# Kernel tuning notes

Measured on AMD Instinct MI355X. Metric: run time of the kernel, lower is better.

The kernel has to match this reference:

```python
import jax, jax.numpy as jnp
from jax import lax
import numpy as np

H = 161  # input_size == hidden_size per the torch module


def _lstm(x, w_ih, w_hh, b_ih, b_hh, reverse):
    """Single-direction LSTM matching torch.nn.LSTM gate order (i, f, g, o).
    x: [B, T, I] -> returns hidden states [B, T, H]."""
    # Precompute the input contribution for all timesteps in one GEMM.
    pre = jnp.einsum('bti,gi->btg', x, w_ih) + b_ih + b_hh  # [B, T, 4H]
    B = x.shape[0]

    def step(carry, p):
        h, c = carry
        gates = p + h @ w_hh.T  # [B, 4H]
        i, f, g, o = jnp.split(gates, 4, axis=-1)
        c = jax.nn.sigmoid(f) * c + jax.nn.sigmoid(i) * jnp.tanh(g)
        h = jax.nn.sigmoid(o) * jnp.tanh(c)
        return (h, c), h

    init = (jnp.zeros((B, H), x.dtype), jnp.zeros((B, H), x.dtype))
    _, hs = lax.scan(step, init, jnp.swapaxes(pre, 0, 1), reverse=reverse)
    return jnp.swapaxes(hs, 0, 1)  # [B, T, H]


def _block(h, p, relu):
    # p = (wih_f, whh_f, bih_f, bhh_f, wih_b, whh_b, bih_b, bhh_b, W, b)
    f = _lstm(h, p[0], p[1], p[2], p[3], reverse=False)
    b = _lstm(h, p[4], p[5], p[6], p[7], reverse=True)
    out = jnp.concatenate([f, b], axis=-1) @ p[8].T + p[9]  # Linear(2H -> H)
    if relu:
        out = jax.nn.relu(out)
    return out + h  # residual


def _forward(x, p1, p2, p3):
    h = _block(x, p1, relu=True)
    h = _block(h, p2, relu=True)
    h = _block(h, p3, relu=False)  # block 3: no ReLU before residual in the torch code
    return h


def setup_inputs() -> dict:
    key = jax.random.key(0)
    ks = iter(jax.random.split(key, 64))
    s = 1.0 / np.sqrt(H)  # torch LSTM/Linear default uniform init scale

    def u(shape):
        return jax.random.uniform(next(ks), shape, jnp.float32, -s, s)

    inp = {"x": jax.random.normal(next(ks), (32, 1000, H), jnp.float32)}
    shapes = [("wih_f", (4 * H, H)), ("whh_f", (4 * H, H)), ("bih_f", (4 * H,)), ("bhh_f", (4 * H,)),
              ("wih_b", (4 * H, H)), ("whh_b", (4 * H, H)), ("bih_b", (4 * H,)), ("bhh_b", (4 * H,)),
              ("W", (H, 2 * H)), ("bl", (H,))]
    for i in (1, 2, 3):
        for nm, sh in shapes:
            inp[f"l{i}_{nm}"] = u(sh)
    return inp


def reference(x,
              l1_wih_f, l1_whh_f, l1_bih_f, l1_bhh_f, l1_wih_b, l1_whh_b, l1_bih_b, l1_bhh_b, l1_W, l1_bl,
              l2_wih_f, l2_whh_f, l2_bih_f, l2_bhh_f, l2_wih_b, l2_whh_b, l2_bih_b, l2_bhh_b, l2_W, l2_bl,
              l3_wih_f, l3_whh_f, l3_bih_f, l3_bhh_f, l3_wih_b, l3_whh_b, l3_bih_b, l3_bhh_b, l3_W, l3_bl):
    p1 = (l1_wih_f, l1_whh_f, l1_bih_f, l1_bhh_f, l1_wih_b, l1_whh_b, l1_bih_b, l1_bhh_b, l1_W, l1_bl)
    p2 = (l2_wih_f, l2_whh_f, l2_bih_f, l2_bhh_f, l2_wih_b, l2_whh_b, l2_bih_b, l2_bhh_b, l2_W, l2_bl)
    p3 = (l3_wih_f, l3_whh_f, l3_bih_f, l3_bhh_f, l3_wih_b, l3_whh_b, l3_bih_b, l3_bhh_b, l3_W, l3_bl)
    return _forward(x, p1, p2, p3)
```

## Files before the change

kernel.cpp:

```cpp
#include <hip/hip_runtime.h>
#include <hip/hip_fp16.h>

#define H 161
#define G4 644
#define BB 32
#define TT 1000
#define M_TOT (BB*TT)
#define KXP 192
#define KLP 352
#define NWIH 1344
#define NPAIR 84
#define NVEC (NPAIR/4)

typedef _Float16 h2_t  __attribute__((ext_vector_type(2)));
typedef _Float16 f16x8 __attribute__((ext_vector_type(8)));
typedef float    f32x4 __attribute__((ext_vector_type(4)));

__device__ __forceinline__ h2_t bc_h2(unsigned int u) {
    return __builtin_bit_cast(h2_t, u);
}

__device__ __forceinline__ float dot2f(h2_t a, h2_t b, float c) {
#if __has_builtin(__builtin_amdgcn_fdot2)
    return __builtin_amdgcn_fdot2(a, b, c, false);
#else
    return c + (float)a[0] * (float)b[0] + (float)a[1] * (float)b[1];
#endif
}

__device__ __forceinline__ float tanh_f(float x) {
    return 1.0f - 2.0f / (__expf(2.0f * x) + 1.0f);
}

__device__ __forceinline__ void bar_lds() {
    __builtin_amdgcn_sched_barrier(0);
    asm volatile("s_waitcnt lgkmcnt(0)" ::: "memory");
    __builtin_amdgcn_s_barrier();
    __builtin_amdgcn_sched_barrier(0);
}

__global__ __launch_bounds__(256) void cvt_x(
    const float* __restrict__ in,
    __half* __restrict__ out)
{
    const int total = M_TOT * KXP;
    for (int idx = blockIdx.x * 256 + threadIdx.x; idx < total;
         idx += gridDim.x * 256) {
        int m = idx / KXP, k = idx - m * KXP;
        float v = (k < H) ? in[(size_t)m * H + k] : (k == H ? 1.f : 0.f);
        out[idx] = __float2half(v);
    }
}

__global__ __launch_bounds__(256) void cvt_wih3(
    const float* __restrict__ wf0, const float* __restrict__ wb0,
    const float* __restrict__ bif0, const float* __restrict__ bhf0,
    const float* __restrict__ bib0, const float* __restrict__ bhb0,
    const float* __restrict__ wf1, const float* __restrict__ wb1,
    const float* __restrict__ bif1, const float* __restrict__ bhf1,
    const float* __restrict__ bib1, const float* __restrict__ bhb1,
    const float* __restrict__ wf2, const float* __restrict__ wb2,
    const float* __restrict__ bif2, const float* __restrict__ bhf2,
    const float* __restrict__ bib2, const float* __restrict__ bhb2,
    __half* __restrict__ out)
{
    const int l = blockIdx.y;
    const float* wf  = (l == 0) ? wf0  : (l == 1) ? wf1  : wf2;
    const float* wb  = (l == 0) ? wb0  : (l == 1) ? wb1  : wb2;
    const float* bif = (l == 0) ? bif0 : (l == 1) ? bif1 : bif2;
    const float* bhf = (l == 0) ? bhf0 : (l == 1) ? bhf1 : bhf2;
    const float* bib = (l == 0) ? bib0 : (l == 1) ? bib1 : bib2;
    const float* bhb = (l == 0) ? bhb0 : (l == 1) ? bhb1 : bhb2;
    __half* o = out + (size_t)l * NWIH * KXP;

    const int total = NWIH * KXP;
    for (int idx = blockIdx.x * 256 + threadIdx.x; idx < total;
         idx += gridDim.x * 256) {
        int n = idx / KXP, k = idx - n * KXP;
        float v = 0.f;
        if (n < G4) {
            v = (k < H) ? wf[(size_t)n * H + k]
                        : (k == H ? bif[n] + bhf[n] : 0.f);
        } else if (n < 2 * G4) {
            int g = n - G4;
            v = (k < H) ? wb[(size_t)g * H + k]
                        : (k == H ? bib[g] + bhb[g] : 0.f);
        }
        o[idx] = __float2half(v);
    }
}

__global__ __launch_bounds__(256) void cvt_W3(
    const float* __restrict__ W0, const float* __restrict__ W1,
    const float* __restrict__ W2,
    __half* __restrict__ out)
{
    const int l = blockIdx.y;
    const float* W = (l == 0) ? W0 : (l == 1) ? W1 : W2;
    __half* o = out + (size_t)l * 192 * KLP;

    const int total = 192 * KLP;
    for (int idx = blockIdx.x * 256 + threadIdx.x; idx < total;
         idx += gridDim.x * 256) {
        int n = idx / KLP, k = idx - n * KLP;
        float v = (n < H && k < 2 * H) ? W[(size_t)n * (2 * H) + k] : 0.f;
        o[idx] = __float2half(v);
    }
}

__global__ __launch_bounds__(256) void pre_mfma(
    const __half* __restrict__ A16,
    const __half* __restrict__ Wih16,
    __half* __restrict__ pre)
{
    const int m0 = blockIdx.x * 64;
    const int n0b = blockIdx.y * 192;
    const int tid = threadIdx.x;
    const int wv = tid >> 6, l = tid & 63;
    const int wm = wv & 1, wn = wv >> 1;
    const int cl = l & 15, kg = l >> 4;

    const __half* ap = A16 + (size_t)(m0 + wm * 32 + cl) * KXP + kg * 8;
    f16x8 xa0[6], xa1[6];
    #pragma unroll
    for (int kt = 0; kt < 6; ++kt) {
        xa0[kt] = *(const f16x8*)(ap + kt * 32);
        xa1[kt] = *(const f16x8*)(ap + 16 * KXP + kt * 32);
    }

    for (int nb = 0; nb < 3; ++nb) {
        const int n0 = n0b + nb * 64;
        const __half* wp = Wih16 + (size_t)(n0 + wn * 32 + cl) * KXP + kg * 8;

        f32x4 acc[2][2] = {};
        #pragma unroll
        for (int kt = 0; kt < 6; ++kt) {
            f16x8 w0 = *(const f16x8*)(wp + kt * 32);
            f16x8 w1 = *(const f16x8*)(wp + 16 * KXP + kt * 32);
            acc[0][0] = __builtin_amdgcn_mfma_f32_16x16x32_f16(w0, xa0[kt], acc[0][0], 0, 0, 0);
            acc[0][1] = __builtin_amdgcn_mfma_f32_16x16x32_f16(w0, xa1[kt], acc[0][1], 0, 0, 0);
            acc[1][0] = __builtin_amdgcn_mfma_f32_16x16x32_f16(w1, xa0[kt], acc[1][0], 0, 0, 0);
            acc[1][1] = __builtin_amdgcn_mfma_f32_16x16x32_f16(w1, xa1[kt], acc[1][1], 0, 0, 0);
        }

        #pragma unroll
        for (int sn = 0; sn < 2; ++sn)
            #pragma unroll
            for (int sm = 0; sm < 2; ++sm) {
                int n = n0 + wn * 32 + sn * 16 + kg * 4;
                int m = m0 + wm * 32 + sm * 16 + cl;
                if (n < 2 * G4) {
                    int d = (n >= G4) ? 1 : 0;
                    int g = n - d * G4;
                    __half2 lo, hi;
                    lo.x = __float2half(acc[sn][sm][0]);
                    lo.y = __float2half(acc[sn][sm][1]);
                    hi.x = __float2half(acc[sn][sm][2]);
                    hi.y = __float2half(acc[sn][sm][3]);
                    __half* dst = pre + ((size_t)d * M_TOT + m) * G4 + g;
                    *(__half2*)dst = lo;
                    *(__half2*)(dst + 2) = hi;
                }
            }
    }
}

__global__ __launch_bounds__(256) void lin_mfma(
    const __half* __restrict__ Hc,
    const __half* __restrict__ W16,
    const float* __restrict__ bl,
    const float* __restrict__ res,
    float* __restrict__ out,
    __half* __restrict__ A16out,
    int relu, int wr_a16)
{
    const int m0 = blockIdx.x * 64, n0 = blockIdx.y * 64;
    const int tid = threadIdx.x;
    const int wv = tid >> 6, l = tid & 63;
    const int wm = wv & 1, wn = wv >> 1;
    const int cl = l & 15, kg = l >> 4;

    const __half* ap = Hc  + (size_t)(m0 + wm * 32 + cl) * KLP + kg * 8;
    const __half* wp = W16 + (size_t)(n0 + wn * 32 + cl) * KLP + kg * 8;

    f32x4 acc[2][2] = {};
    #pragma unroll
    for (int kt = 0; kt < 11; ++kt) {
        f16x8 w0 = *(const f16x8*)(wp + kt * 32);
        f16x8 w1 = *(const f16x8*)(wp + 16 * KLP + kt * 32);
        f16x8 x0 = *(const f16x8*)(ap + kt * 32);
        f16x8 x1 = *(const f16x8*)(ap + 16 * KLP + kt * 32);
        acc[0][0] = __builtin_amdgcn_mfma_f32_16x16x32_f16(w0, x0, acc[0][0], 0, 0, 0);
        acc[0][1] = __builtin_amdgcn_mfma_f32_16x16x32_f16(w0, x1, acc[0][1], 0, 0, 0);
        acc[1][0] = __builtin_amdgcn_mfma_f32_16x16x32_f16(w1, x0, acc[1][0], 0, 0, 0);
        acc[1][1] = __builtin_amdgcn_mfma_f32_16x16x32_f16(w1, x1, acc[1][1], 0, 0, 0);
    }

    #pragma unroll
    for (int sn = 0; sn < 2; ++sn)
        #pragma unroll
        for (int sm = 0; sm < 2; ++sm) {
            int nb = n0 + wn * 32 + sn * 16 + kg * 4;
            int m  = m0 + wm * 32 + sm * 16 + cl;
            #pragma unroll
            for (int r = 0; r < 4; ++r) {
                int n = nb + r;
                if (n < H) {
                    float v = acc[sn][sm][r] + bl[n];
                    if (relu) v = fmaxf(v, 0.f);
                    v += res[(size_t)m * H + n];
                    out[(size_t)m * H + n] = v;
                    if (wr_a16)
                        A16out[(size_t)m * KXP + n] = __float2half(v);
                }
            }
        }
}

__global__ __launch_bounds__(704, 3) void lstm_scan(
    const __half* __restrict__ pre,
    const float* __restrict__ whh_f,
    const float* __restrict__ whh_b,
    __half* __restrict__ hcat)
{
    const int b = blockIdx.x;
    const int d = blockIdx.y;
    const int tid = threadIdx.x;
    const float* whh = d ? whh_b : whh_f;

    __shared__ __align__(16) unsigned int h_sh[NPAIR];
    __shared__ float gate_sh[G4];

    const bool active = tid < G4;
    h2_t w[NPAIR];
    if (active) {
        const float* row = whh + (size_t)tid * H;
        #pragma unroll
        for (int i = 0; i < NPAIR; ++i) {
            float w0 = (2 * i < H) ? row[2 * i] : 0.f;
            float w1 = (2 * i + 1 < H) ? row[2 * i + 1] : 0.f;
            h2_t v; v[0] = (_Float16)w0; v[1] = (_Float16)w1;
            w[i] = v;
        }
    }
    if (tid < NPAIR) h_sh[tid] = 0u;
    float c = 0.f;
    const __half* pb = pre + ((size_t)d * M_TOT + (size_t)b * TT) * G4;
    const bool is_g_gate = (tid >= 2 * H) && (tid < 3 * H);

    int t0 = d ? (TT - 1) : 0;
    __half pc = __half(0.0f);
    if (active) pc = pb[(long long)t0 * G4 + tid];
    __syncthreads();

    for (int ttt = 0; ttt < TT; ++ttt) {
        int t = d ? (TT - 1 - ttt) : ttt;
        int tn = d ? (t - 1) : (t + 1);
        __half pn = __half(0.0f);
        if (active) pn = pb[(long long)tn * G4 + tid];

        if (active) {
            float a0 = 0.f, a1 = 0.f, a2 = 0.f, a3 = 0.f;
            const uint4* hv = (const uint4*)h_sh;
            #pragma unroll
            for (int i = 0; i < NVEC; ++i) {
                uint4 hh = hv[i];
                a0 = dot2f(w[4 * i + 0], bc_h2(hh.x), a0);
                a1 = dot2f(w[4 * i + 1], bc_h2(hh.y), a1);
                a2 = dot2f(w[4 * i + 2], bc_h2(hh.z), a2);
                a3 = dot2f(w[4 * i + 3], bc_h2(hh.w), a3);
            }
            float acc = __half2float(pc) + (a0 + a1) + (a2 + a3);
            float xs = is_g_gate ? (acc + acc) : acc;
            float s = 1.0f / (1.0f + __expf(-xs));
            gate_sh[tid] = is_g_gate ? (s + s - 1.0f) : s;
        }
        bar_lds();
        if (tid < H) {
            float ig = gate_sh[tid];
            float fg = gate_sh[tid + H];
            float gg = gate_sh[tid + 2 * H];
            float og = gate_sh[tid + 3 * H];
            c = fg * c + ig * gg;
            float h = og * tanh_f(c);
            __half h16 = __float2half(h);
            hcat[((size_t)b * TT + t) * KLP + (size_t)d * H + tid] = h16;
            ((__half*)h_sh)[tid] = h16;
        }
        bar_lds();
        pc = pn;
    }
}

extern "C" void kernel_launch(void* const* d_in, const int* in_sizes, int n_in,
                              void* d_out, int out_size, void* d_ws, size_t ws_size,
                              hipStream_t stream) {
    const float* x = (const float*)d_in[0];

    char* ws = (char*)d_ws;
    __half* pre    = (__half*)ws;
    __half* hcat16 = (__half*)(ws + (size_t)2 * M_TOT * G4 * 2);
    __half* A16    = (__half*)((char*)hcat16 + (size_t)M_TOT * KLP * 2);
    __half* wih3   = (__half*)((char*)A16 + (size_t)M_TOT * KXP * 2);
    __half* W3     = (__half*)((char*)wih3 + (size_t)3 * NWIH * KXP * 2);
    float*  bufA   = (float*)((char*)W3 + (size_t)3 * 192 * KLP * 2);
    float*  bufB   = bufA + (size_t)M_TOT * H;

    const float* const* p0 = (const float* const*)(d_in + 1);
    const float* const* p1 = (const float* const*)(d_in + 11);
    const float* const* p2 = (const float* const*)(d_in + 21);

    hipMemsetAsync(hcat16, 0, (size_t)M_TOT * KLP * sizeof(__half), stream);
    cvt_x<<<2048, 256, 0, stream>>>(x, A16);
    cvt_wih3<<<dim3(256, 3), 256, 0, stream>>>(
        p0[0], p0[4], p0[2], p0[3], p0[6], p0[7],
        p1[0], p1[4], p1[2], p1[3], p1[6], p1[7],
        p2[0], p2[4], p2[2], p2[3], p2[6], p2[7], wih3);
    cvt_W3<<<dim3(64, 3), 256, 0, stream>>>(p0[8], p1[8], p2[8], W3);

    const float* const* ps[3] = {p0, p1, p2};
    const float* cur = x;
    float* outs[3] = {bufA, bufB, (float*)d_out};

    for (int l = 0; l < 3; ++l) {
        const float* const* p = ps[l];
        pre_mfma<<<dim3(M_TOT / 64, 7), 256, 0, stream>>>(
            A16, wih3 + (size_t)l * NWIH * KXP, pre);
        lstm_scan<<<dim3(32, 2), 704, 0, stream>>>(pre, p[1], p[5], hcat16);
        lin_mfma<<<dim3(M_TOT / 64, 3), 256, 0, stream>>>(
            hcat16, W3 + (size_t)l * 192 * KLP, p[9], cur, outs[l], A16,
            (l < 2) ? 1 : 0, (l < 2) ? 1 : 0);
        cur = outs[l];
    }
}
```

Baseline: 3.478 ms.

## Interleave gates per quad with DPP exchange and double-buffer hidden state

Remaps LSTM scan threads so the four gates of each hidden unit sit in adjacent lanes of a quad. DPP quad permutes then share gate activations, so the cell update no longer goes through an LDS gate array. The hidden state is double-buffered, which cuts the per-step barriers from two to one, and the pre-activation prefetch is deepened to two steps. The cost is a larger block (704 threads, all computing, with padded rows) and redundant cell computation in three of every four lanes.

```diff
diff --git a/kernel.cpp b/kernel.cpp
--- a/kernel.cpp
+++ b/kernel.cpp
@@ -30,6 +30,13 @@
 
 __device__ __forceinline__ float tanh_f(float x) {
     return 1.0f - 2.0f / (__expf(2.0f * x) + 1.0f);
+}
+
+template<int CTRL>
+__device__ __forceinline__ float dpp_qp(float x) {
+    int y = __builtin_amdgcn_update_dpp(0, __builtin_bit_cast(int, x),
+                                        CTRL, 0xF, 0xF, true);
+    return __builtin_bit_cast(float, y);
 }
 
 __device__ __forceinline__ void bar_lds() {
@@ -226,15 +233,19 @@
     const int b = blockIdx.x;
     const int d = blockIdx.y;
     const int tid = threadIdx.x;
+    const int l = tid & 63, wv = tid >> 6;
+    const int gate = l & 3;
+    const int hid = wv * 16 + (l >> 2);
+    const int hidc = (hid < H) ? hid : (H - 1);
+    const bool writer = (gate == 0) && (hid < H);
+    const bool is_g = (gate == 2);
     const float* whh = d ? whh_b : whh_f;
 
-    __shared__ __align__(16) unsigned int h_sh[NPAIR];
-    __shared__ float gate_sh[G4];
-
-    const bool active = tid < G4;
+    __shared__ __align__(16) unsigned int h_sh[2][NPAIR];
+
     h2_t w[NPAIR];
-    if (active) {
-        const float* row = whh + (size_t)tid * H;
+    {
+        const float* row = whh + (size_t)(gate * H + hidc) * H;
         #pragma unroll
         for (int i = 0; i < NPAIR; ++i) {
             float w0 = (2 * i < H) ? row[2 * i] : 0.f;
@@ -243,53 +254,56 @@
             w[i] = v;
         }
     }
-    if (tid < NPAIR) h_sh[tid] = 0u;
+    if (tid < 2 * NPAIR) ((unsigned int*)h_sh)[tid] = 0u;
+
     float c = 0.f;
-    const __half* pb = pre + ((size_t)d * M_TOT + (size_t)b * TT) * G4;
-    const bool is_g_gate = (tid >= 2 * H) && (tid < 3 * H);
-
-    int t0 = d ? (TT - 1) : 0;
-    __half pc = __half(0.0f);
-    if (active) pc = pb[(long long)t0 * G4 + tid];
+    const __half* pb = pre + ((size_t)d * M_TOT + (size_t)b * TT) * G4
+                           + gate * H + hidc;
+
+    #define LDP(tt_) ({ int tc_ = ((tt_) < TT) ? (tt_) : (TT - 1);          \
+                        int t_  = d ? (TT - 1 - tc_) : tc_;                 \
+                        pb[(size_t)t_ * G4]; })
+
+    __half p0 = LDP(0), p1 = LDP(1);
     __syncthreads();
 
-    for (int ttt = 0; ttt < TT; ++ttt) {
-        int t = d ? (TT - 1 - ttt) : ttt;
-        int tn = d ? (t - 1) : (t + 1);
-        __half pn = __half(0.0f);
-        if (active) pn = pb[(long long)tn * G4 + tid];
-
-        if (active) {
-            float a0 = 0.f, a1 = 0.f, a2 = 0.f, a3 = 0.f;
-            const uint4* hv = (const uint4*)h_sh;
-            #pragma unroll
-            for (int i = 0; i < NVEC; ++i) {
-                uint4 hh = hv[i];
-                a0 = dot2f(w[4 * i + 0], bc_h2(hh.x), a0);
-                a1 = dot2f(w[4 * i + 1], bc_h2(hh.y), a1);
-                a2 = dot2f(w[4 * i + 2], bc_h2(hh.z), a2);
-                a3 = dot2f(w[4 * i + 3], bc_h2(hh.w), a3);
-            }
-            float acc = __half2float(pc) + (a0 + a1) + (a2 + a3);
-            float xs = is_g_gate ? (acc + acc) : acc;
-            float s = 1.0f / (1.0f + __expf(-xs));
-            gate_sh[tid] = is_g_gate ? (s + s - 1.0f) : s;
-        }
-        bar_lds();
-        if (tid < H) {
-            float ig = gate_sh[tid];
-            float fg = gate_sh[tid + H];
-            float gg = gate_sh[tid + 2 * H];
-            float og = gate_sh[tid + 3 * H];
-            c = fg * c + ig * gg;
-            float h = og * tanh_f(c);
-            __half h16 = __float2half(h);
-            hcat[((size_t)b * TT + t) * KLP + (size_t)d * H + tid] = h16;
-            ((__half*)h_sh)[tid] = h16;
-        }
-        bar_lds();
-        pc = pn;
-    }
+    #define STEP(TTT, PJ, BUF) {                                            \
+        int t = d ? (TT - 1 - (TTT)) : (TTT);                               \
+        float pc = __half2float(PJ);                                        \
+        PJ = LDP((TTT) + 2);                    \
+        float a0 = 0.f, a1 = 0.f, a2 = 0.f, a3 = 0.f;                       \
+        const uint4* hv = (const uint4*)h_sh[BUF];                          \
+        _Pragma("unroll")                                                   \
+        for (int i = 0; i < NVEC; ++i) {                                    \
+            uint4 hh = hv[i];                                               \
+            a0 = dot2f(w[4 * i + 0], bc_h2(hh.x), a0);                      \
+            a1 = dot2f(w[4 * i + 1], bc_h2(hh.y), a1);                      \
+            a2 = dot2f(w[4 * i + 2], bc_h2(hh.z), a2);                      \
+            a3 = dot2f(w[4 * i + 3], bc_h2(hh.w), a3);                      \
+        }                                                                   \
+        float acc = pc + (a0 + a1) + (a2 + a3);                             \
+        float xs = is_g ? (acc + acc) : acc;                                \
+        float s = 1.0f / (1.0f + __expf(-xs));                              \
+        float act = is_g ? (s + s - 1.0f) : s;                              \
+        float fA = dpp_qp<0xB1>(act);           \
+        float gA = dpp_qp<0x4E>(act);           \
+        float oA = dpp_qp<0x1B>(act);           \
+        c = fA * c + act * gA;               \
+        float hval = oA * tanh_f(c);                                        \
+        if (writer) {                                                       \
+            __half h16 = __float2half(hval);                                \
+            hcat[((size_t)b * TT + t) * KLP + (size_t)d * H + hid] = h16;   \
+            ((__half*)h_sh[(BUF) ^ 1])[hid] = h16;                          \
+        }                                                                   \
+        bar_lds();                                                          \
+    }
+
+    for (int base = 0; base < TT; base += 2) {
+        STEP(base,     p0, 0)
+        STEP(base + 1, p1, 1)
+    }
+    #undef STEP
+    #undef LDP
 }
 
 extern "C" void kernel_launch(void* const* d_in, const int* in_sizes, int n_in,
```

Result: no change. 3.507 ms (+0.8%).
